# Kernel tuning notes

Hardware: AMD Instinct MI355X
Metric: run time of the kernel (lower is better)

Reference implementation:

```python
import jax, jax.numpy as jnp
import numpy as np

B, T, C, H = 4, 2048, 1024, 16

def setup_inputs() -> dict:
    key = jax.random.key(0)
    ks = jax.random.split(key, 5)
    s = 1.0 / np.sqrt(C)
    return {
        "x": jax.random.normal(ks[0], (B, T, C), jnp.float32),
        "Wq": jax.random.normal(ks[1], (C, C), jnp.float32) * s,
        "bq": jnp.zeros((C,), jnp.float32),
        "Wk": jax.random.normal(ks[2], (C, C), jnp.float32) * s,
        "bk": jnp.zeros((C,), jnp.float32),
        "Wv": jax.random.normal(ks[3], (C, C), jnp.float32) * s,
        "bv": jnp.zeros((C,), jnp.float32),
        "Wp": jax.random.normal(ks[4], (C, C), jnp.float32) * s,
        "bp": jnp.zeros((C,), jnp.float32),
    }

def reference(x, Wq, bq, Wk, bk, Wv, bv, Wp, bp):
    b, t, c = x.shape
    hd = c // H  # head dim
    # projections; W stored as [in, out] (torch Linear transposed)
    q = (x @ Wq + bq).reshape(b, t, H, hd).transpose(0, 2, 1, 3)  # [B,H,T,hd]
    k = (x @ Wk + bk).reshape(b, t, H, hd).transpose(0, 2, 1, 3)
    v = (x @ Wv + bv).reshape(b, t, H, hd).transpose(0, 2, 1, 3)
    att = jnp.einsum("bhqd,bhkd->bhqk", q, k) * (1.0 / np.sqrt(hd))
    causal = jnp.tril(jnp.ones((t, t), bool))
    att = jnp.where(causal, att, -jnp.inf)
    att = jax.nn.softmax(att, axis=-1)
    y = jnp.einsum("bhqk,bhkd->bhqd", att, v)  # [B,H,T,hd]
    y = y.transpose(0, 2, 1, 3).reshape(b, t, c)
    return y @ Wp + bp
```

## Files before the change

### kernel.cpp

```cpp
#include <hip/hip_runtime.h>
#include <stdint.h>

#define B_  4
#define T_  2048
#define C_  1024
#define H_  16
#define HD_ 64
#define M_  (B_*T_)

typedef __attribute__((ext_vector_type(8)))  __bf16 bf16x8;
typedef __attribute__((ext_vector_type(4)))  float  f32x4;
typedef __attribute__((ext_vector_type(16))) float  f32x16;
typedef __attribute__((ext_vector_type(4)))  unsigned int u32x4;

#define QSCALE 0.18033688011112042f

__device__ __forceinline__ unsigned short f2bf(float f) {
    union { float f; unsigned int u; } v; v.f = f;
    unsigned int r = v.u + 0x7fffu + ((v.u >> 16) & 1u);
    return (unsigned short)(r >> 16);
}
__device__ __forceinline__ unsigned int pack2(float a, float b) {
    return (unsigned int)f2bf(a) | ((unsigned int)f2bf(b) << 16);
}
__device__ __forceinline__ void gload16(const void* g, void* l) {
    __builtin_amdgcn_global_load_lds(
        (const __attribute__((address_space(1))) unsigned int*)(uintptr_t)g,
        (__attribute__((address_space(3))) unsigned int*)(unsigned int)(uintptr_t)l,
        16, 0, 0);
}

__global__ __launch_bounds__(256) void k_cvt_x(const float* __restrict__ x,
                                               unsigned short* __restrict__ xb, int n8) {
    int i = blockIdx.x * blockDim.x + threadIdx.x;
    if (i >= n8) return;
    const float4* p = (const float4*)x + (size_t)i * 2;
    float4 a = p[0], b = p[1];
    u32x4 o = { pack2(a.x, a.y), pack2(a.z, a.w), pack2(b.x, b.y), pack2(b.z, b.w) };
    *(u32x4*)(xb + (size_t)i * 8) = o;
}

__global__ __launch_bounds__(256) void k_transpose_cvt(const float* __restrict__ src,
                                                       unsigned short* __restrict__ dst,
                                                       int rows, int cols) {
    __shared__ float tile[32][33];
    int c0 = blockIdx.x * 32, r0 = blockIdx.y * 32;
    int tx = threadIdx.x, ty = threadIdx.y;
    for (int i = 0; i < 4; i++)
        tile[ty + i * 8][tx] = src[(size_t)(r0 + ty + i * 8) * cols + c0 + tx];
    __syncthreads();
    for (int i = 0; i < 4; i++)
        dst[(size_t)(c0 + ty + i * 8) * rows + r0 + tx] = f2bf(tile[tx][ty + i * 8]);
}

template<int MODE>
__global__ __launch_bounds__(256) void k_gemm(
    const unsigned short* __restrict__ A,
    const unsigned short* __restrict__ Bt,
    const float* __restrict__ bias0, const float* __restrict__ bias1,
    const float* __restrict__ bias2,
    unsigned short* __restrict__ qo, unsigned short* __restrict__ ko,
    unsigned short* __restrict__ vto, float* __restrict__ outf)
{
    const int K = C_;
    __shared__ __align__(16) unsigned short As[128][32];
    __shared__ __align__(16) unsigned short Bs[128][32];
    int m0 = blockIdx.x * 128, n0 = blockIdx.y * 128;
    int t = threadIdx.x, w = t >> 6, l = t & 63;
    int wm = w >> 1, wn = w & 1;
    int lg = l >> 4, lr = l & 15;

    f32x4 acc[4][4];
    for (int i = 0; i < 4; i++) for (int j = 0; j < 4; j++)
        acc[i][j] = (f32x4){0.f, 0.f, 0.f, 0.f};

    int arow = w * 16 + (l >> 2);
    int acol = (l & 3) * 8;
    char* asb = (char*)&As[0][0] + w * 1024 + l * 16;
    char* bsb = (char*)&Bs[0][0] + w * 1024 + l * 16;

    for (int k0 = 0; k0 < K; k0 += 32) {
        __syncthreads();
        #pragma unroll
        for (int j = 0; j < 2; j++) {
            gload16(A  + (size_t)(m0 + j * 64 + arow) * K + k0 + acol, asb + j * 4096);
            gload16(Bt + (size_t)(n0 + j * 64 + arow) * K + k0 + acol, bsb + j * 4096);
        }
        __syncthreads();
        bf16x8 af[4], bfr[4];
        #pragma unroll
        for (int i = 0; i < 4; i++) af[i]  = *(const bf16x8*)(&As[wm * 64 + i * 16 + lr][lg * 8]);
        #pragma unroll
        for (int j = 0; j < 4; j++) bfr[j] = *(const bf16x8*)(&Bs[wn * 64 + j * 16 + lr][lg * 8]);
        #pragma unroll
        for (int i = 0; i < 4; i++)
            #pragma unroll
            for (int j = 0; j < 4; j++)
                acc[i][j] = __builtin_amdgcn_mfma_f32_16x16x32_bf16(af[i], bfr[j], acc[i][j], 0, 0, 0);
    }

    #pragma unroll
    for (int i = 0; i < 4; i++) {
        #pragma unroll
        for (int j = 0; j < 4; j++) {
            int mrow = m0 + wm * 64 + i * 16 + lg * 4;
            int ncol = n0 + wn * 64 + j * 16 + lr;
            if (MODE == 0) {
                int sel = ncol >> 10, nc = ncol & 1023;
                int hh = nc >> 6, dd = nc & 63;
                const float* bp = (sel == 0) ? bias0 : (sel == 1) ? bias1 : bias2;
                float bvv = bp[nc];
                for (int r = 0; r < 4; r++) {
                    int mm = mrow + r;
                    int bb = mm >> 11, tt = mm & (T_ - 1);
                    float v = acc[i][j][r] + bvv;
                    if (sel == 0)      qo[((size_t)((bb * H_ + hh) * T_) + tt) * HD_ + dd] = f2bf(v * QSCALE);
                    else if (sel == 1) ko[((size_t)((bb * H_ + hh) * T_) + tt) * HD_ + dd] = f2bf(v);
                    else               vto[((size_t)((bb * H_ + hh) * HD_) + dd) * T_ + tt] = f2bf(v);
                }
            } else {
                float bvv = bias0[ncol];
                for (int r = 0; r < 4; r++)
                    outf[(size_t)(mrow + r) * C_ + ncol] = acc[i][j][r] + bvv;
            }
        }
    }
}

__device__ __forceinline__ void sm_pack(f32x16& st, bool mask, int lq, int lh,
                                        float& mi, float& li, f32x16& o0, f32x16& o1,
                                        unsigned int* pw)
{
    if (mask) {
        #pragma unroll
        for (int r = 0; r < 16; r++) {
            int key = (r & 3) + 8 * (r >> 2) + 4 * lh;
            if (key > lq) st[r] = -1e30f;
        }
    }
    float tm[8];
    #pragma unroll
    for (int i = 0; i < 8; i++) tm[i] = fmaxf(st[2 * i], st[2 * i + 1]);
    #pragma unroll
    for (int i = 0; i < 4; i++) tm[i] = fmaxf(tm[i], tm[i + 4]);
    float tmax = fmaxf(fmaxf(tm[0], tm[2]), fmaxf(tm[1], tm[3]));
    tmax = fmaxf(tmax, __shfl_xor(tmax, 32));
    if (!__all(tmax <= mi)) {
        float mnew = fmaxf(mi, tmax);
        float fac = exp2f(mi - mnew);
        mi = mnew;
        li *= fac;
        #pragma unroll
        for (int r = 0; r < 16; r++) { o0[r] *= fac; o1[r] *= fac; }
    }
    #pragma unroll
    for (int r = 0; r < 16; r++) st[r] = exp2f(st[r] - mi);
    float rsum[8];
    #pragma unroll
    for (int i = 0; i < 8; i++) rsum[i] = st[2 * i] + st[2 * i + 1];
    #pragma unroll
    for (int i = 0; i < 4; i++) rsum[i] += rsum[i + 4];
    float rs = (rsum[0] + rsum[2]) + (rsum[1] + rsum[3]);
    rs += __shfl_xor(rs, 32);
    li += rs;
    #pragma unroll
    for (int kc = 0; kc < 2; kc++) {
        unsigned int a0, a1, b0, b1;
        asm("v_cvt_pk_bf16_f32 %0, %1, %2" : "=v"(a0) : "v"(st[kc*8+0]), "v"(st[kc*8+1]));
        asm("v_cvt_pk_bf16_f32 %0, %1, %2" : "=v"(a1) : "v"(st[kc*8+2]), "v"(st[kc*8+3]));
        asm("v_cvt_pk_bf16_f32 %0, %1, %2" : "=v"(b0) : "v"(st[kc*8+4]), "v"(st[kc*8+5]));
        asm("v_cvt_pk_bf16_f32 %0, %1, %2" : "=v"(b1) : "v"(st[kc*8+6]), "v"(st[kc*8+7]));
        asm volatile("v_permlane32_swap_b32 %0, %1" : "+v"(a0), "+v"(b0));
        asm volatile("v_permlane32_swap_b32 %0, %1" : "+v"(a1), "+v"(b1));
        pw[kc*4+0] = a0; pw[kc*4+1] = a1; pw[kc*4+2] = b0; pw[kc*4+3] = b1;
    }
}

__device__ __forceinline__ void pv_step(const unsigned int* pw, const bf16x8* vc,
                                        f32x16& o0, f32x16& o1)
{
    #pragma unroll
    for (int kc = 0; kc < 2; kc++) {
        union { u32x4 u; bf16x8 v; } pb;
        pb.u = (u32x4){pw[kc*4+0], pw[kc*4+1], pw[kc*4+2], pw[kc*4+3]};
        o0 = __builtin_amdgcn_mfma_f32_32x32x16_bf16(vc[kc*2],     pb.v, o0, 0, 0, 0);
        o1 = __builtin_amdgcn_mfma_f32_32x32x16_bf16(vc[kc*2 + 1], pb.v, o1, 0, 0, 0);
    }
}

__device__ __forceinline__ void attn_writeout(unsigned int (*otw)[36],
                                              const f32x16& o0, const f32x16& o1, float li,
                                              int lq, int lh, int l,
                                              unsigned short* dst)
{
    float inv = 1.f / li;
    #pragma unroll
    for (int r = 0; r < 16; r += 2) {
        int dh = ((r & 3) + 8 * (r >> 2) + 4 * lh) >> 1;
        otw[lq][dh]      = pack2(o0[r] * inv, o0[r + 1] * inv);
        otw[lq][16 + dh] = pack2(o1[r] * inv, o1[r + 1] * inv);
    }
    asm volatile("s_waitcnt lgkmcnt(0)" ::: "memory");
    __builtin_amdgcn_sched_barrier(0);
    #pragma unroll
    for (int i = 0; i < 4; i++) {
        int c = i * 64 + l;
        int q = c >> 3, ch = c & 7;
        u32x4 rv = *(const u32x4*)(&otw[q][ch * 4]);
        *(u32x4*)(dst + (size_t)q * C_ + ch * 8) = rv;
    }
}

__device__ __forceinline__ void stage_kv(const unsigned short* kp, const unsigned short* vp,
                                         char* lds, int kt, int tid)
{
    int r = tid >> 3, sl = tid & 7;
    #pragma unroll
    for (int c = 0; c < 2; c++) {
        int row = c * 32 + r;
        gload16(kp + ((size_t)(kt * 64 + row)) * HD_ + ((sl ^ (row & 7)) * 8),
                lds + c * 4096 + tid * 16);
    }
    #pragma unroll
    for (int c = 0; c < 2; c++) {
        int d = c * 32 + r;
        gload16(vp + (size_t)d * T_ + kt * 64 + ((sl ^ (d & 7)) * 8),
                lds + 8192 + c * 4096 + tid * 16);
    }
}

__global__ __launch_bounds__(256, 2) void k_attn(
    const unsigned short* __restrict__ qb,
    const unsigned short* __restrict__ kb,
    const unsigned short* __restrict__ vtb,
    unsigned short* __restrict__ yb)
{
    __shared__ __align__(16) char smem[32768];
    int bh = blockIdx.x;
    int x  = blockIdx.y;
    int h = bh & (H_ - 1), b = bh >> 4;
    int tid = threadIdx.x, w = tid >> 6, l = tid & 63;
    int lq = l & 31, lh = l >> 5;
    int p = x * 4 + w;
    int qtA = p, qtB = 63 - p;
    int qbA = qtA * 32, qbB = qtB * 32;
    int nt = 32 - 2 * x;

    const unsigned short* qp = qb  + (size_t)bh * T_ * HD_;
    const unsigned short* kp = kb  + (size_t)bh * T_ * HD_;
    const unsigned short* vp = vtb + (size_t)bh * HD_ * T_;

    bf16x8 qA[4], qB[4];
    #pragma unroll
    for (int dc = 0; dc < 4; dc++) {
        qA[dc] = *(const bf16x8*)(qp + (size_t)(qbA + lq) * HD_ + dc * 16 + lh * 8);
        qB[dc] = *(const bf16x8*)(qp + (size_t)(qbB + lq) * HD_ + dc * 16 + lh * 8);
    }

    f32x16 oA0, oA1, oB0, oB1;
    #pragma unroll
    for (int r = 0; r < 16; r++) { oA0[r] = 0.f; oA1[r] = 0.f; oB0[r] = 0.f; oB1[r] = 0.f; }
    float miA = 12.f, liA = 0.f, miB = 12.f, liB = 0.f;

    stage_kv(kp, vp, smem,         0, tid);
    stage_kv(kp, vp, smem + 16384, 1, tid);

    for (int t = 0; t < nt; t++) {
        if (t < nt - 1) asm volatile("s_waitcnt vmcnt(4)" ::: "memory");
        else            asm volatile("s_waitcnt vmcnt(0)" ::: "memory");
        __builtin_amdgcn_s_barrier();
        __builtin_amdgcn_sched_barrier(0);
        const unsigned short* Kb = (const unsigned short*)(smem + (t & 1) * 16384);
        const unsigned short* Vb = Kb + 4096;

        #pragma unroll
        for (int s = 0; s < 2; s++) {
            int kt32 = 2 * t + s;
            if (kt32 > qtB) break;
            bool doA = (kt32 <= qtA);

            bf16x8 kc[4], vc[4];
            #pragma unroll
            for (int dc = 0; dc < 4; dc++) {
                int row = s * 32 + lq;
                kc[dc] = *(const bf16x8*)(Kb + row * 64 + (((dc * 2 + lh) ^ (row & 7)) * 8));
            }
            #pragma unroll
            for (int vi = 0; vi < 4; vi++) {
                int d = lq + (vi & 1) * 32;
                int slot = (s * 4 + (vi >> 1) * 2 + lh) ^ (d & 7);
                vc[vi] = *(const bf16x8*)(Vb + d * 64 + slot * 8);
            }

            f32x16 stA, stB;
            #pragma unroll
            for (int r = 0; r < 16; r++) { stA[r] = 0.f; stB[r] = 0.f; }
            __builtin_amdgcn_s_setprio(1);
            #pragma unroll
            for (int dc = 0; dc < 4; dc++) {
                stB = __builtin_amdgcn_mfma_f32_32x32x16_bf16(kc[dc], qB[dc], stB, 0, 0, 0);
                if (doA)
                    stA = __builtin_amdgcn_mfma_f32_32x32x16_bf16(kc[dc], qA[dc], stA, 0, 0, 0);
            }
            __builtin_amdgcn_s_setprio(0);

            unsigned int pwA[8], pwB[8];
            sm_pack(stB, (kt32 == qtB), lq, lh, miB, liB, oB0, oB1, pwB);
            if (doA) sm_pack(stA, (kt32 == qtA), lq, lh, miA, liA, oA0, oA1, pwA);
            __builtin_amdgcn_s_setprio(1);
            pv_step(pwB, vc, oB0, oB1);
            if (doA) pv_step(pwA, vc, oA0, oA1);
            __builtin_amdgcn_s_setprio(0);
        }

        __builtin_amdgcn_s_barrier();
        __builtin_amdgcn_sched_barrier(0);
        if (t + 2 < nt) stage_kv(kp, vp, smem + (t & 1) * 16384, t + 2, tid);
    }

    unsigned int (*otw)[36] = (unsigned int (*)[36])(smem + w * 4608);
    unsigned short* dstA = yb + (size_t)(b * T_ + qbA) * C_ + h * HD_;
    unsigned short* dstB = yb + (size_t)(b * T_ + qbB) * C_ + h * HD_;
    attn_writeout(otw, oA0, oA1, liA, lq, lh, l, dstA);
    attn_writeout(otw, oB0, oB1, liB, lq, lh, l, dstB);
}

extern "C" void kernel_launch(void* const* d_in, const int* in_sizes, int n_in,
                              void* d_out, int out_size, void* d_ws, size_t ws_size,
                              hipStream_t stream) {
    const float* x  = (const float*)d_in[0];
    const float* Wq = (const float*)d_in[1];
    const float* bq = (const float*)d_in[2];
    const float* Wk = (const float*)d_in[3];
    const float* bk = (const float*)d_in[4];
    const float* Wv = (const float*)d_in[5];
    const float* bv = (const float*)d_in[6];
    const float* Wp = (const float*)d_in[7];
    const float* bp = (const float*)d_in[8];
    float* out = (float*)d_out;

    char* ws = (char*)d_ws;
    unsigned short* xb    = (unsigned short*)(ws);
    unsigned short* wqkvt = (unsigned short*)(ws + (16u << 20));
    unsigned short* wpt   = (unsigned short*)(ws + (22u << 20));
    unsigned short* qbuf  = (unsigned short*)(ws + (24u << 20));
    unsigned short* kbuf  = (unsigned short*)(ws + (40u << 20));
    unsigned short* vtbuf = (unsigned short*)(ws + (56u << 20));
    unsigned short* ybuf  = (unsigned short*)(ws + (72u << 20));

    int n8 = M_ * C_ / 8;
    k_cvt_x<<<(n8 + 255) / 256, 256, 0, stream>>>(x, xb, n8);

    dim3 tb(32, 8);
    dim3 tg(32, 32);
    k_transpose_cvt<<<tg, tb, 0, stream>>>(Wq, wqkvt,              C_, C_);
    k_transpose_cvt<<<tg, tb, 0, stream>>>(Wk, wqkvt + (1u << 20), C_, C_);
    k_transpose_cvt<<<tg, tb, 0, stream>>>(Wv, wqkvt + (2u << 20), C_, C_);
    k_transpose_cvt<<<tg, tb, 0, stream>>>(Wp, wpt,                C_, C_);

    k_gemm<0><<<dim3(M_ / 128, 3 * C_ / 128), 256, 0, stream>>>(
        xb, wqkvt, bq, bk, bv, qbuf, kbuf, vtbuf, nullptr);

    k_attn<<<dim3(64, 8), 256, 0, stream>>>(qbuf, kbuf, vtbuf, ybuf);

    k_gemm<1><<<dim3(M_ / 128, C_ / 128), 256, 0, stream>>>(
        ybuf, wpt, bp, nullptr, nullptr, nullptr, nullptr, nullptr, out);
}
```

Measured before the change: 290.8 us.

## Replace GEMMs with 256x256 tiled, 8-wave, double-buffered swizzled LDS pipeline

Rewrites both projection GEMMs as a 512-thread kernel computing 256x256 output tiles with a K-step of 64. Global loads are double-buffered into 128KB of XOR-swizzled LDS and interleaved with MFMA quadrants, using explicit vmcnt waits, raw barriers and setprio. The goal is to hide global-load latency, avoid LDS bank conflicts and raise arithmetic intensity compared with the old 128x128 tile, which synchronized on every 32-wide K step. In exchange it uses many more registers and most of the LDS, and the grid has far fewer blocks (only 128 for the output projection), which risks poor CU occupancy.

```diff
diff --git a/kernel.cpp b/kernel.cpp
--- a/kernel.cpp
+++ b/kernel.cpp
@@ -53,8 +53,51 @@
         dst[(size_t)(c0 + ty + i * 8) * rows + r0 + tx] = f2bf(tile[tx][ty + i * 8]);
 }
 
+#define SWZ(rr, cb) ((rr) * 128 + ((cb) ^ (((rr) & 7) << 4)))
+
+#define DS_A(slot, mh) { \
+  _Pragma("unroll") for (int fi = 0; fi < 4; fi++) { \
+    int rrow = wm * 64 + fi * 16 + lr; \
+    const char* base = lds + (slot) * 32768 + (mh) * 16384; \
+    aR[fi][0] = *(const bf16x8*)(base + SWZ(rrow, lg * 16)); \
+    aR[fi][1] = *(const bf16x8*)(base + SWZ(rrow, 64 + lg * 16)); \
+  } }
+
+#define DS_B(slot, nh) { \
+  _Pragma("unroll") for (int fj = 0; fj < 2; fj++) { \
+    int rrow = wn * 32 + fj * 16 + lr; \
+    const char* base = lds + 65536 + (slot) * 32768 + (nh) * 16384; \
+    bR[fj][0] = *(const bf16x8*)(base + SWZ(rrow, lg * 16)); \
+    bR[fj][1] = *(const bf16x8*)(base + SWZ(rrow, 64 + lg * 16)); \
+  } }
+
+#define MMA16(mh, nh) { \
+  asm volatile("s_waitcnt lgkmcnt(0)" ::: "memory"); \
+  __builtin_amdgcn_sched_barrier(0); \
+  __builtin_amdgcn_s_setprio(1); \
+  _Pragma("unroll") for (int ks = 0; ks < 2; ks++) \
+    _Pragma("unroll") for (int fi = 0; fi < 4; fi++) \
+      _Pragma("unroll") for (int fj = 0; fj < 2; fj++) \
+        acc[(mh)*4+fi][(nh)*2+fj] = __builtin_amdgcn_mfma_f32_16x16x32_bf16( \
+            aR[fi][ks], bR[fj][ks], acc[(mh)*4+fi][(nh)*2+fj], 0, 0, 0); \
+  __builtin_amdgcn_s_setprio(0); \
+}
+
+#define STAGE(isB, slot, hf, kt) { \
+  const unsigned short* gp = ((isB) ? Bt + (size_t)(n0 + (hf)*128) * K \
+                                    : A  + (size_t)(m0 + (hf)*128) * K) + (kt) * 64; \
+  char* dstp = lds + ((isB) ? 65536 : 0) + (slot) * 32768 + (hf) * 16384; \
+  _Pragma("unroll") for (int li = 0; li < 2; li++) { \
+    int L = tid * 16 + li * 8192; \
+    int rr = L >> 7; \
+    int cb = (L & 127) ^ ((rr & 7) << 4); \
+    gload16(gp + (size_t)rr * K + (cb >> 1), dstp + L); \
+  } }
+
+#define BAR() __builtin_amdgcn_s_barrier()
+
 template<int MODE>
-__global__ __launch_bounds__(256) void k_gemm(
+__global__ __launch_bounds__(512, 2) void k_gemm8(
     const unsigned short* __restrict__ A,
     const unsigned short* __restrict__ Bt,
     const float* __restrict__ bias0, const float* __restrict__ bias1,
@@ -63,53 +106,68 @@
     unsigned short* __restrict__ vto, float* __restrict__ outf)
 {
     const int K = C_;
-    __shared__ __align__(16) unsigned short As[128][32];
-    __shared__ __align__(16) unsigned short Bs[128][32];
-    int m0 = blockIdx.x * 128, n0 = blockIdx.y * 128;
-    int t = threadIdx.x, w = t >> 6, l = t & 63;
-    int wm = w >> 1, wn = w & 1;
+    __shared__ __align__(16) char lds[131072];
+    int m0 = blockIdx.x * 256, n0 = blockIdx.y * 256;
+    int tid = threadIdx.x, wid = tid >> 6, l = tid & 63;
+    int wm = wid >> 2, wn = wid & 3;
     int lg = l >> 4, lr = l & 15;
 
-    f32x4 acc[4][4];
-    for (int i = 0; i < 4; i++) for (int j = 0; j < 4; j++)
-        acc[i][j] = (f32x4){0.f, 0.f, 0.f, 0.f};
-
-    int arow = w * 16 + (l >> 2);
-    int acol = (l & 3) * 8;
-    char* asb = (char*)&As[0][0] + w * 1024 + l * 16;
-    char* bsb = (char*)&Bs[0][0] + w * 1024 + l * 16;
-
-    for (int k0 = 0; k0 < K; k0 += 32) {
-        __syncthreads();
+    f32x4 acc[8][4];
+    #pragma unroll
+    for (int i = 0; i < 8; i++)
         #pragma unroll
-        for (int j = 0; j < 2; j++) {
-            gload16(A  + (size_t)(m0 + j * 64 + arow) * K + k0 + acol, asb + j * 4096);
-            gload16(Bt + (size_t)(n0 + j * 64 + arow) * K + k0 + acol, bsb + j * 4096);
-        }
-        __syncthreads();
-        bf16x8 af[4], bfr[4];
-        #pragma unroll
-        for (int i = 0; i < 4; i++) af[i]  = *(const bf16x8*)(&As[wm * 64 + i * 16 + lr][lg * 8]);
-        #pragma unroll
-        for (int j = 0; j < 4; j++) bfr[j] = *(const bf16x8*)(&Bs[wn * 64 + j * 16 + lr][lg * 8]);
-        #pragma unroll
-        for (int i = 0; i < 4; i++)
-            #pragma unroll
-            for (int j = 0; j < 4; j++)
-                acc[i][j] = __builtin_amdgcn_mfma_f32_16x16x32_bf16(af[i], bfr[j], acc[i][j], 0, 0, 0);
-    }
-
-    #pragma unroll
-    for (int i = 0; i < 4; i++) {
+        for (int j = 0; j < 4; j++) acc[i][j] = (f32x4){0.f, 0.f, 0.f, 0.f};
+
+    bf16x8 aR[4][2], bR[2][2];
+
+    STAGE(0, 0, 0, 0); STAGE(1, 0, 0, 0); STAGE(1, 0, 1, 0); STAGE(0, 0, 1, 0);
+    STAGE(0, 1, 0, 1); STAGE(1, 1, 1, 1); STAGE(0, 1, 1, 1);
+    asm volatile("s_waitcnt vmcnt(6)" ::: "memory");
+    BAR();
+
+    for (int it = 0; it < 8; it++) {
+        int t1  = 2 * it + 1;
+        int nx0 = (2 * it + 2) & 15, nx1 = (2 * it + 3) & 15;
+        STAGE(1, 1, 0, t1);
+        DS_A(0, 0); DS_B(0, 0);
+        BAR(); MMA16(0, 0); BAR();
+        STAGE(0, 0, 0, nx0);
+        DS_B(0, 1);
+        BAR(); MMA16(0, 1); BAR();
+        STAGE(1, 0, 1, nx0);
+        DS_A(0, 1);
+        BAR(); MMA16(1, 1); BAR();
+        STAGE(0, 0, 1, nx0);
+        DS_B(0, 0);
+        asm volatile("s_waitcnt vmcnt(6)" ::: "memory");
+        BAR(); MMA16(1, 0); BAR();
+        STAGE(1, 0, 0, nx0);
+        DS_A(1, 0); DS_B(1, 0);
+        BAR(); MMA16(0, 0); BAR();
+        STAGE(0, 1, 0, nx1);
+        DS_B(1, 1);
+        BAR(); MMA16(0, 1); BAR();
+        STAGE(1, 1, 1, nx1);
+        DS_A(1, 1);
+        BAR(); MMA16(1, 1); BAR();
+        STAGE(0, 1, 1, nx1);
+        DS_B(1, 0);
+        asm volatile("s_waitcnt vmcnt(6)" ::: "memory");
+        BAR(); MMA16(1, 0); BAR();
+    }
+
+    #pragma unroll
+    for (int i = 0; i < 8; i++) {
         #pragma unroll
         for (int j = 0; j < 4; j++) {
-            int mrow = m0 + wm * 64 + i * 16 + lg * 4;
-            int ncol = n0 + wn * 64 + j * 16 + lr;
+            int mrow = m0 + (i >> 2) * 128 + wm * 64 + (i & 3) * 16 + lg * 4;
+            int ncol = n0 + (j >> 1) * 128 + wn * 32 + (j & 1) * 16 + lr;
             if (MODE == 0) {
                 int sel = ncol >> 10, nc = ncol & 1023;
                 int hh = nc >> 6, dd = nc & 63;
                 const float* bp = (sel == 0) ? bias0 : (sel == 1) ? bias1 : bias2;
                 float bvv = bp[nc];
+                #pragma unroll
                 for (int r = 0; r < 4; r++) {
                     int mm = mrow + r;
                     int bb = mm >> 11, tt = mm & (T_ - 1);
@@ -120,6 +178,7 @@
                 }
             } else {
                 float bvv = bias0[ncol];
+                #pragma unroll
                 for (int r = 0; r < 4; r++)
                     outf[(size_t)(mrow + r) * C_ + ncol] = acc[i][j][r] + bvv;
             }
@@ -212,20 +271,20 @@
 }
 
 __device__ __forceinline__ void stage_kv(const unsigned short* kp, const unsigned short* vp,
-                                         char* lds, int kt, int tid)
+                                         char* ldsp, int kt, int tid)
 {
     int r = tid >> 3, sl = tid & 7;
     #pragma unroll
     for (int c = 0; c < 2; c++) {
         int row = c * 32 + r;
         gload16(kp + ((size_t)(kt * 64 + row)) * HD_ + ((sl ^ (row & 7)) * 8),
-                lds + c * 4096 + tid * 16);
+                ldsp + c * 4096 + tid * 16);
     }
     #pragma unroll
     for (int c = 0; c < 2; c++) {
         int d = c * 32 + r;
         gload16(vp + (size_t)d * T_ + kt * 64 + ((sl ^ (d & 7)) * 8),
-                lds + 8192 + c * 4096 + tid * 16);
+                ldsp + 8192 + c * 4096 + tid * 16);
     }
 }
 
@@ -358,11 +417,11 @@
     k_transpose_cvt<<<tg, tb, 0, stream>>>(Wv, wqkvt + (2u << 20), C_, C_);
     k_transpose_cvt<<<tg, tb, 0, stream>>>(Wp, wpt,                C_, C_);
 
-    k_gemm<0><<<dim3(M_ / 128, 3 * C_ / 128), 256, 0, stream>>>(
+    k_gemm8<0><<<dim3(M_ / 256, 3 * C_ / 256), 512, 0, stream>>>(
         xb, wqkvt, bq, bk, bv, qbuf, kbuf, vtbuf, nullptr);
 
     k_attn<<<dim3(64, 8), 256, 0, stream>>>(qbuf, kbuf, vtbuf, ybuf);
 
-    k_gemm<1><<<dim3(M_ / 128, C_ / 128), 256, 0, stream>>>(
+    k_gemm8<1><<<dim3(M_ / 256, C_ / 256), 512, 0, stream>>>(
         ybuf, wpt, bp, nullptr, nullptr, nullptr, nullptr, nullptr, out);
 }
```

Result: slower. 310.9 us (+6.9%).
